# Optimization experiments

Hardware: AMD Instinct MI355X
Metric: run time of the kernel (lower is better)

The kernel has to match this reference:

```python
import jax, jax.numpy as jnp
import numpy as np

NUM_GRAPHS = 64
EPS = 1e-6


def setup_inputs() -> dict:
    key = jax.random.key(0)
    ks = jax.random.split(key, 16)
    S, B, IN, H, N, P_IN, P_OUT = 256, 64, 3, 128, 1_000_000, 8, 32
    src = jax.random.normal(ks[0], (S, B, IN), dtype=jnp.float32)
    src_len = jnp.maximum(jax.random.randint(ks[1], (B,), 0, S + 1), 1).astype(jnp.int32)
    node_x = jax.random.normal(ks[2], (N, H), dtype=jnp.float32)
    # w is a 0/1 node validity mask in the original (float)
    node_w = (jax.random.uniform(ks[3], (N,)) < 0.9).astype(jnp.float32)
    graph_ids = jnp.sort(jax.random.randint(ks[4], (N,), 0, NUM_GRAPHS)).astype(jnp.int32)
    pro_features = jax.random.normal(ks[5], (B, P_IN), dtype=jnp.float32)
    s_in = 1.0 / np.sqrt(IN)
    s_h = 1.0 / np.sqrt(H)
    s_p = 1.0 / np.sqrt(P_IN)
    s_c = 1.0 / np.sqrt(H + P_OUT)
    W_in = jax.random.uniform(ks[6], (IN, H), minval=-s_in, maxval=s_in)
    b_in = jax.random.uniform(ks[7], (H,), minval=-s_in, maxval=s_in)
    W_pred = jax.random.uniform(ks[8], (H, 1), minval=-s_h, maxval=s_h)
    b_pred = jax.random.uniform(ks[9], (1,), minval=-s_h, maxval=s_h)
    W_extra = jax.random.uniform(ks[10], (P_IN, P_OUT), minval=-s_p, maxval=s_p)
    b_extra = jax.random.uniform(ks[11], (P_OUT,), minval=-s_p, maxval=s_p)
    W_hid = jax.random.uniform(ks[12], (P_OUT + H, H), minval=-s_c, maxval=s_c)
    b_hid = jax.random.uniform(ks[13], (H,), minval=-s_c, maxval=s_c)
    return {"src": src, "src_len": src_len, "node_x": node_x, "node_w": node_w,
            "graph_ids": graph_ids, "pro_features": pro_features,
            "W_in": W_in, "b_in": b_in, "W_pred": W_pred, "b_pred": b_pred,
            "W_extra": W_extra, "b_extra": b_extra, "W_hid": W_hid, "b_hid": b_hid}


def mask_graph_log_softmax(lg, w, graph_ids):
    # lg: [N], w: [N], graph_ids: [N] sorted segment ids -> per-graph masked softmax, then log
    maxes = jax.ops.segment_max(lg, graph_ids, num_segments=NUM_GRAPHS)
    x_exp = jnp.exp(lg - maxes[graph_ids]) * w
    x_sum = jax.ops.segment_sum(x_exp, graph_ids, num_segments=NUM_GRAPHS)
    pred = x_exp / (x_sum[graph_ids] + EPS)
    return jnp.log(jnp.clip(pred, EPS, 1.0))


def reference(src, src_len, node_x, node_w, graph_ids, pro_features,
              W_in, b_in, W_pred, b_pred, W_extra, b_extra, W_hid, b_hid):
    S, B = src.shape[0], src.shape[1]
    # mask2d[i, t] = 1 for t < src_len[i]
    mask2d = (jnp.arange(S)[None, :] < src_len[:, None]).astype(src.dtype)  # [B, S]
    h = jnp.tanh(0.0) + src @ W_in + b_in  # [S, B, H]  (fc_in; transformer treated as identity)
    # zero out padded timesteps, then mean over dim 0 (torch.mean divides by S)
    outputs = h * mask2d.T[:, :, None]  # [S, B, H]
    hidden = jnp.mean(outputs, axis=0, keepdims=True)  # [1, B, H]
    # graph segment softmax on node scores
    lg = (node_x @ W_pred + b_pred)[:, 0]  # [N]
    lg_out = mask_graph_log_softmax(lg, node_w, graph_ids)[:, None]  # [N, 1]
    # pro feature fusion
    extra_emb = jnp.tanh(pro_features @ W_extra + b_extra)[None]  # [1, B, P_OUT]
    hidden = jnp.tanh(jnp.concatenate((extra_emb, hidden), axis=2) @ W_hid + b_hid)  # [1, B, H]
    return outputs, hidden, lg_out
```

## Files before the change

kernel.cpp:

```cpp
#include <hip/hip_runtime.h>

#define S_DIM 256
#define B_DIM 64
#define IN_DIM 3
#define H_DIM 128
#define N_NODES 1000000
#define NM1 (N_NODES - 1)
#define P_INF 8
#define P_OUTF 32
#define NUM_GRAPHS 64
#define EPSF 1e-6f

#define OUT_OUTPUTS 0
#define OUT_HIDDEN (S_DIM * B_DIM * H_DIM)
#define OUT_LG (OUT_HIDDEN + B_DIM * H_DIM)

#define NBLK 1024
#define TPB 512
#define RPB 977
#define GSTEP 64
#define SG_SLOTS 6

#define WS_HIDPART 0
#define WS_TBLV (16 * B_DIM * H_DIM)
#define WS_TBLG (WS_TBLV + NBLK * SG_SLOTS)

__global__ void __launch_bounds__(TPB, 8)
main_kernel(const float* __restrict__ src, const int* __restrict__ src_len,
            const float* __restrict__ W_in, const float* __restrict__ b_in,
            const float* __restrict__ node_x, const float* __restrict__ W_pred,
            const float* __restrict__ b_pred, const float* __restrict__ node_w,
            const int* __restrict__ gids,
            float* __restrict__ outputs, float* __restrict__ hid_partial,
            float* __restrict__ lg, float* __restrict__ tblV, int* __restrict__ tblG) {
    __shared__ float sg[SG_SLOTS];
    const int tid = threadIdx.x;
    const int blk = blockIdx.x;
    if (tid < SG_SLOTS) sg[tid] = 0.0f;

    if (blk < 256) {
        int b = blk & 63;
        int chunk = blk >> 6;
        int h = tid & 127;
        int sq = tid >> 7;
        float w0 = W_in[h], w1 = W_in[H_DIM + h], w2 = W_in[2 * H_DIM + h];
        float bi = b_in[h];
        int len = src_len[b];
        float facc = 0.0f;
        int s0 = chunk * 64 + sq * 16;
        for (int s = s0; s < s0 + 16; ++s) {
            const float* sp = src + ((size_t)s * B_DIM + b) * IN_DIM;
            float v = fmaf(sp[0], w0, fmaf(sp[1], w1, fmaf(sp[2], w2, bi)));
            v = (s < len) ? v : 0.0f;
            outputs[((size_t)s * B_DIM + b) * H_DIM + h] = v;
            facc += v;
        }
        hid_partial[((size_t)(chunk * 4 + sq) * B_DIM + b) * H_DIM + h] = facc;
    }
    __syncthreads();

    const int start = blk * RPB;
    const int bend = min(start + RPB, N_NODES);
    const int gfirst = gids[min(start, NM1)];
    const int w = tid >> 6;
    const int lane = tid & 63;
    const int p = lane & 7;
    const int rloc = lane >> 3;

    float4 wch0 = ((const float4*)W_pred)[p];
    float4 wch1 = ((const float4*)W_pred)[p + 8];
    float4 wch2 = ((const float4*)W_pred)[p + 16];
    float4 wch3 = ((const float4*)W_pred)[p + 24];
    const float bp = b_pred[0];

    int curg = -1;
    float acc = 0.0f;

    for (int r0 = start + w * 8; r0 < bend; r0 += GSTEP) {
        int sidx = min(r0 + p, NM1);
        float wv = node_w[sidx];
        int gv = gids[sidx];
        int xrow = min(r0 + rloc, NM1);
        const float4* xb = (const float4*)(node_x + (size_t)xrow * H_DIM);
        float4 x0 = xb[p];
        float4 x1 = xb[p + 8];
        float4 x2 = xb[p + 16];
        float4 x3 = xb[p + 24];
        float s = x0.x * wch0.x + x0.y * wch0.y + x0.z * wch0.z + x0.w * wch0.w;
        s += x1.x * wch1.x + x1.y * wch1.y + x1.z * wch1.z + x1.w * wch1.w;
        s += x2.x * wch2.x + x2.y * wch2.y + x2.z * wch2.z + x2.w * wch2.w;
        s += x3.x * wch3.x + x3.y * wch3.y + x3.z * wch3.z + x3.w * wch3.w;
        s += __shfl_xor(s, 1);
        s += __shfl_xor(s, 2);
        s += __shfl_xor(s, 4);
        float rowsum = __shfl(s, p * 8);
        int myrow = r0 + p;
        if (lane < 8 && myrow < bend) {
            float score = rowsum + bp;
            lg[myrow] = score;
            float xe = __expf(score) * wv;
            if (gv != curg) {
                if (curg >= 0) atomicAdd(&sg[min(curg - gfirst, SG_SLOTS - 1)], acc);
                curg = gv;
                acc = 0.0f;
            }
            acc += xe;
        }
    }
    if (curg >= 0) atomicAdd(&sg[min(curg - gfirst, SG_SLOTS - 1)], acc);
    __syncthreads();
    if (tid < SG_SLOTS) tblV[blk * SG_SLOTS + tid] = sg[tid];
    if (tid == 0) tblG[blk] = gfirst;
}

#define LGOUT_BLOCKS 977

__global__ void __launch_bounds__(256)
finish_kernel(const float* __restrict__ tblV, const int* __restrict__ tblG,
              float* __restrict__ lg, const int* __restrict__ gids,
              const float* __restrict__ node_w,
              const float* __restrict__ pro, const float* __restrict__ W_extra,
              const float* __restrict__ b_extra, const float* __restrict__ W_hid,
              const float* __restrict__ b_hid, const float* __restrict__ hid_partial,
              float* __restrict__ hidden_out) {
    const int tid = threadIdx.x;
    const int blk = blockIdx.x;

    if (blk >= LGOUT_BLOCKS) {
        int b = blk - LGOUT_BLOCKS;
        __shared__ float sh[P_OUTF + H_DIM];
        if (tid < P_OUTF) {
            float a = b_extra[tid];
            #pragma unroll
            for (int k = 0; k < P_INF; ++k) a += pro[b * P_INF + k] * W_extra[k * P_OUTF + tid];
            sh[tid] = tanhf(a);
        }
        if (tid < H_DIM) {
            float m = 0.0f;
            #pragma unroll
            for (int c = 0; c < 16; ++c) m += hid_partial[((size_t)c * B_DIM + b) * H_DIM + tid];
            sh[P_OUTF + tid] = m * (1.0f / S_DIM);
        }
        __syncthreads();
        if (tid < H_DIM) {
            float a = b_hid[tid];
            #pragma unroll 8
            for (int k = 0; k < P_OUTF + H_DIM; ++k) a += sh[k] * W_hid[k * H_DIM + tid];
            hidden_out[(size_t)b * H_DIM + tid] = tanhf(a);
        }
        return;
    }

    __shared__ float gsum[NUM_GRAPHS];
    if (tid < NUM_GRAPHS) gsum[tid] = 0.0f;
    __syncthreads();
    {
        int cg2 = -1;
        float a = 0.0f;
        for (int b = tid * (NBLK / 256); b < (tid + 1) * (NBLK / 256); ++b) {
            int gf = tblG[b];
            #pragma unroll
            for (int slot = 0; slot < SG_SLOTS; ++slot) {
                float v = tblV[b * SG_SLOTS + slot];
                if (v != 0.0f) {
                    int g = min(gf + slot, NUM_GRAPHS - 1);
                    if (g != cg2) {
                        if (cg2 >= 0) atomicAdd(&gsum[cg2], a);
                        cg2 = g;
                        a = 0.0f;
                    }
                    a += v;
                }
            }
        }
        if (cg2 >= 0) atomicAdd(&gsum[cg2], a);
    }
    __syncthreads();

    int n4 = blk * 256 + tid;
    if (n4 >= N_NODES / 4) return;
    float4 l = ((const float4*)lg)[n4];
    float4 w = ((const float4*)node_w)[n4];
    int4 g = ((const int4*)gids)[n4];
    float4 r;
    r.x = __logf(fminf(fmaxf(__expf(l.x) * w.x / (gsum[g.x] + EPSF), EPSF), 1.0f));
    r.y = __logf(fminf(fmaxf(__expf(l.y) * w.y / (gsum[g.y] + EPSF), EPSF), 1.0f));
    r.z = __logf(fminf(fmaxf(__expf(l.z) * w.z / (gsum[g.z] + EPSF), EPSF), 1.0f));
    r.w = __logf(fminf(fmaxf(__expf(l.w) * w.w / (gsum[g.w] + EPSF), EPSF), 1.0f));
    ((float4*)lg)[n4] = r;
}

extern "C" void kernel_launch(void* const* d_in, const int* in_sizes, int n_in,
                              void* d_out, int out_size, void* d_ws, size_t ws_size,
                              hipStream_t stream) {
    const float* src      = (const float*)d_in[0];
    const int*   src_len  = (const int*)d_in[1];
    const float* node_x   = (const float*)d_in[2];
    const float* node_w   = (const float*)d_in[3];
    const int*   gids     = (const int*)d_in[4];
    const float* pro      = (const float*)d_in[5];
    const float* W_in     = (const float*)d_in[6];
    const float* b_in     = (const float*)d_in[7];
    const float* W_pred   = (const float*)d_in[8];
    const float* b_pred   = (const float*)d_in[9];
    const float* W_extra  = (const float*)d_in[10];
    const float* b_extra  = (const float*)d_in[11];
    const float* W_hid    = (const float*)d_in[12];
    const float* b_hid    = (const float*)d_in[13];

    float* out = (float*)d_out;
    float* outputs = out + OUT_OUTPUTS;
    float* hidden  = out + OUT_HIDDEN;
    float* lg      = out + OUT_LG;

    float* ws = (float*)d_ws;
    float* hid_partial = ws + WS_HIDPART;
    float* tblV = ws + WS_TBLV;
    int*   tblG = (int*)(ws + WS_TBLG);

    main_kernel<<<NBLK, TPB, 0, stream>>>(src, src_len, W_in, b_in,
                                          node_x, W_pred, b_pred, node_w, gids,
                                          outputs, hid_partial, lg, tblV, tblG);

    finish_kernel<<<LGOUT_BLOCKS + B_DIM, 256, 0, stream>>>(tblV, tblG, lg, gids, node_w,
                                                            pro, W_extra, b_extra, W_hid,
                                                            b_hid, hid_partial, hidden);
}
```

Before: 123.8 us.

## Fuse main and finish kernels into one cooperative kernel with grid sync

Merges the scoring/projection kernel and the normalization/hidden kernel into a single cooperative launch separated by a grid-wide barrier. The grid size now comes from an occupancy query, and the last 64 blocks compute the hidden output. The node_x reads and the lg reads and writes switch to nontemporal loads and stores. This removes the second launch and inter-kernel gap, at the cost of a grid sync and a simpler per-value atomic reduction of the per-block graph sums.

```diff
diff --git a/kernel.cpp b/kernel.cpp
--- a/kernel.cpp
+++ b/kernel.cpp
@@ -1,4 +1,7 @@
 #include <hip/hip_runtime.h>
+#include <hip/hip_cooperative_groups.h>
+
+namespace cg = cooperative_groups;
 
 #define S_DIM 256
 #define B_DIM 64
@@ -6,6 +9,7 @@
 #define H_DIM 128
 #define N_NODES 1000000
 #define NM1 (N_NODES - 1)
+#define N4_TOTAL (N_NODES / 4)
 #define P_INF 8
 #define P_OUTF 32
 #define NUM_GRAPHS 64
@@ -15,27 +19,35 @@
 #define OUT_HIDDEN (S_DIM * B_DIM * H_DIM)
 #define OUT_LG (OUT_HIDDEN + B_DIM * H_DIM)
 
-#define NBLK 1024
 #define TPB 512
-#define RPB 977
-#define GSTEP 64
+#define NBLK_MAX 1024
 #define SG_SLOTS 6
 
 #define WS_HIDPART 0
 #define WS_TBLV (16 * B_DIM * H_DIM)
-#define WS_TBLG (WS_TBLV + NBLK * SG_SLOTS)
+#define WS_TBLG (WS_TBLV + NBLK_MAX * SG_SLOTS)
+
+typedef float f4v __attribute__((ext_vector_type(4)));
+typedef int i4v __attribute__((ext_vector_type(4)));
 
 __global__ void __launch_bounds__(TPB, 8)
-main_kernel(const float* __restrict__ src, const int* __restrict__ src_len,
-            const float* __restrict__ W_in, const float* __restrict__ b_in,
-            const float* __restrict__ node_x, const float* __restrict__ W_pred,
-            const float* __restrict__ b_pred, const float* __restrict__ node_w,
-            const int* __restrict__ gids,
-            float* __restrict__ outputs, float* __restrict__ hid_partial,
-            float* __restrict__ lg, float* __restrict__ tblV, int* __restrict__ tblG) {
+fused_kernel(const float* __restrict__ src, const int* __restrict__ src_len,
+             const float* __restrict__ W_in, const float* __restrict__ b_in,
+             const float* __restrict__ node_x, const float* __restrict__ W_pred,
+             const float* __restrict__ b_pred, const float* __restrict__ node_w,
+             const int* __restrict__ gids,
+             const float* __restrict__ pro, const float* __restrict__ W_extra,
+             const float* __restrict__ b_extra, const float* __restrict__ W_hid,
+             const float* __restrict__ b_hid,
+             float* __restrict__ outputs, float* __restrict__ hidden_out,
+             float* __restrict__ lg, float* __restrict__ hid_partial,
+             float* __restrict__ tblV, int* __restrict__ tblG, int rpb) {
     __shared__ float sg[SG_SLOTS];
+    __shared__ float gsum[NUM_GRAPHS];
+    __shared__ float sh[P_OUTF + H_DIM];
     const int tid = threadIdx.x;
     const int blk = blockIdx.x;
+    const int nblk = gridDim.x;
     if (tid < SG_SLOTS) sg[tid] = 0.0f;
 
     if (blk < 256) {
@@ -59,33 +71,33 @@
     }
     __syncthreads();
 
-    const int start = blk * RPB;
-    const int bend = min(start + RPB, N_NODES);
+    const int start = blk * rpb;
+    const int bend = min(start + rpb, N_NODES);
     const int gfirst = gids[min(start, NM1)];
     const int w = tid >> 6;
     const int lane = tid & 63;
     const int p = lane & 7;
     const int rloc = lane >> 3;
 
-    float4 wch0 = ((const float4*)W_pred)[p];
-    float4 wch1 = ((const float4*)W_pred)[p + 8];
-    float4 wch2 = ((const float4*)W_pred)[p + 16];
-    float4 wch3 = ((const float4*)W_pred)[p + 24];
+    f4v wch0 = ((const f4v*)W_pred)[p];
+    f4v wch1 = ((const f4v*)W_pred)[p + 8];
+    f4v wch2 = ((const f4v*)W_pred)[p + 16];
+    f4v wch3 = ((const f4v*)W_pred)[p + 24];
     const float bp = b_pred[0];
 
     int curg = -1;
     float acc = 0.0f;
 
-    for (int r0 = start + w * 8; r0 < bend; r0 += GSTEP) {
+    for (int r0 = start + w * 8; r0 < bend; r0 += 64) {
         int sidx = min(r0 + p, NM1);
         float wv = node_w[sidx];
         int gv = gids[sidx];
         int xrow = min(r0 + rloc, NM1);
-        const float4* xb = (const float4*)(node_x + (size_t)xrow * H_DIM);
-        float4 x0 = xb[p];
-        float4 x1 = xb[p + 8];
-        float4 x2 = xb[p + 16];
-        float4 x3 = xb[p + 24];
+        const f4v* xb = (const f4v*)(node_x + (size_t)xrow * H_DIM);
+        f4v x0 = __builtin_nontemporal_load(xb + p);
+        f4v x1 = __builtin_nontemporal_load(xb + p + 8);
+        f4v x2 = __builtin_nontemporal_load(xb + p + 16);
+        f4v x3 = __builtin_nontemporal_load(xb + p + 24);
         float s = x0.x * wch0.x + x0.y * wch0.y + x0.z * wch0.z + x0.w * wch0.w;
         s += x1.x * wch1.x + x1.y * wch1.y + x1.z * wch1.z + x1.w * wch1.w;
         s += x2.x * wch2.x + x2.y * wch2.y + x2.z * wch2.z + x2.w * wch2.w;
@@ -97,7 +109,7 @@
         int myrow = r0 + p;
         if (lane < 8 && myrow < bend) {
             float score = rowsum + bp;
-            lg[myrow] = score;
+            __builtin_nontemporal_store(score, &lg[myrow]);
             float xe = __expf(score) * wv;
             if (gv != curg) {
                 if (curg >= 0) atomicAdd(&sg[min(curg - gfirst, SG_SLOTS - 1)], acc);
@@ -111,24 +123,11 @@
     __syncthreads();
     if (tid < SG_SLOTS) tblV[blk * SG_SLOTS + tid] = sg[tid];
     if (tid == 0) tblG[blk] = gfirst;
-}
-
-#define LGOUT_BLOCKS 977
-
-__global__ void __launch_bounds__(256)
-finish_kernel(const float* __restrict__ tblV, const int* __restrict__ tblG,
-              float* __restrict__ lg, const int* __restrict__ gids,
-              const float* __restrict__ node_w,
-              const float* __restrict__ pro, const float* __restrict__ W_extra,
-              const float* __restrict__ b_extra, const float* __restrict__ W_hid,
-              const float* __restrict__ b_hid, const float* __restrict__ hid_partial,
-              float* __restrict__ hidden_out) {
-    const int tid = threadIdx.x;
-    const int blk = blockIdx.x;
-
-    if (blk >= LGOUT_BLOCKS) {
-        int b = blk - LGOUT_BLOCKS;
-        __shared__ float sh[P_OUTF + H_DIM];
+
+    cg::this_grid().sync();
+
+    if (blk >= nblk - 64) {
+        int b = blk - (nblk - 64);
         if (tid < P_OUTF) {
             float a = b_extra[tid];
             #pragma unroll
@@ -151,43 +150,32 @@
         return;
     }
 
-    __shared__ float gsum[NUM_GRAPHS];
+    if (blk * TPB >= N4_TOTAL) return;
+
     if (tid < NUM_GRAPHS) gsum[tid] = 0.0f;
     __syncthreads();
-    {
-        int cg2 = -1;
-        float a = 0.0f;
-        for (int b = tid * (NBLK / 256); b < (tid + 1) * (NBLK / 256); ++b) {
-            int gf = tblG[b];
-            #pragma unroll
-            for (int slot = 0; slot < SG_SLOTS; ++slot) {
-                float v = tblV[b * SG_SLOTS + slot];
-                if (v != 0.0f) {
-                    int g = min(gf + slot, NUM_GRAPHS - 1);
-                    if (g != cg2) {
-                        if (cg2 >= 0) atomicAdd(&gsum[cg2], a);
-                        cg2 = g;
-                        a = 0.0f;
-                    }
-                    a += v;
-                }
-            }
-        }
-        if (cg2 >= 0) atomicAdd(&gsum[cg2], a);
-    }
-    __syncthreads();
-
-    int n4 = blk * 256 + tid;
-    if (n4 >= N_NODES / 4) return;
-    float4 l = ((const float4*)lg)[n4];
-    float4 w = ((const float4*)node_w)[n4];
-    int4 g = ((const int4*)gids)[n4];
-    float4 r;
-    r.x = __logf(fminf(fmaxf(__expf(l.x) * w.x / (gsum[g.x] + EPSF), EPSF), 1.0f));
-    r.y = __logf(fminf(fmaxf(__expf(l.y) * w.y / (gsum[g.y] + EPSF), EPSF), 1.0f));
-    r.z = __logf(fminf(fmaxf(__expf(l.z) * w.z / (gsum[g.z] + EPSF), EPSF), 1.0f));
-    r.w = __logf(fminf(fmaxf(__expf(l.w) * w.w / (gsum[g.w] + EPSF), EPSF), 1.0f));
-    ((float4*)lg)[n4] = r;
+    for (int b = tid; b < nblk; b += TPB) {
+        int gf = tblG[b];
+        #pragma unroll
+        for (int slot = 0; slot < SG_SLOTS; ++slot) {
+            float v = tblV[b * SG_SLOTS + slot];
+            if (v != 0.0f) atomicAdd(&gsum[min(gf + slot, NUM_GRAPHS - 1)], v);
+        }
+    }
+    __syncthreads();
+
+    int stride = (nblk - 64) * TPB;
+    for (int n4 = blk * TPB + tid; n4 < N4_TOTAL; n4 += stride) {
+        f4v l = __builtin_nontemporal_load((const f4v*)lg + n4);
+        f4v wq = __builtin_nontemporal_load((const f4v*)node_w + n4);
+        i4v g = __builtin_nontemporal_load((const i4v*)gids + n4);
+        f4v r;
+        r.x = __logf(fminf(fmaxf(__expf(l.x) * wq.x / (gsum[g.x] + EPSF), EPSF), 1.0f));
+        r.y = __logf(fminf(fmaxf(__expf(l.y) * wq.y / (gsum[g.y] + EPSF), EPSF), 1.0f));
+        r.z = __logf(fminf(fmaxf(__expf(l.z) * wq.z / (gsum[g.z] + EPSF), EPSF), 1.0f));
+        r.w = __logf(fminf(fmaxf(__expf(l.w) * wq.w / (gsum[g.w] + EPSF), EPSF), 1.0f));
+        __builtin_nontemporal_store(r, (f4v*)lg + n4);
+    }
 }
 
 extern "C" void kernel_launch(void* const* d_in, const int* in_sizes, int n_in,
@@ -218,11 +206,22 @@
     float* tblV = ws + WS_TBLV;
     int*   tblG = (int*)(ws + WS_TBLG);
 
-    main_kernel<<<NBLK, TPB, 0, stream>>>(src, src_len, W_in, b_in,
-                                          node_x, W_pred, b_pred, node_w, gids,
-                                          outputs, hid_partial, lg, tblV, tblG);
-
-    finish_kernel<<<LGOUT_BLOCKS + B_DIM, 256, 0, stream>>>(tblV, tblG, lg, gids, node_w,
-                                                            pro, W_extra, b_extra, W_hid,
-                                                            b_hid, hid_partial, hidden);
+    int nb_per_cu = 0;
+    hipOccupancyMaxActiveBlocksPerMultiprocessor(&nb_per_cu, (const void*)fused_kernel,
+                                                 TPB, 0);
+    int nblk = nb_per_cu * 256;
+    if (nblk > NBLK_MAX) nblk = NBLK_MAX;
+    if (nblk < 320) nblk = 320;
+    int rpb = (N_NODES + nblk - 1) / nblk;
+
+    void* args[] = {
+        (void*)&src, (void*)&src_len, (void*)&W_in, (void*)&b_in,
+        (void*)&node_x, (void*)&W_pred, (void*)&b_pred, (void*)&node_w,
+        (void*)&gids, (void*)&pro, (void*)&W_extra, (void*)&b_extra,
+        (void*)&W_hid, (void*)&b_hid,
+        (void*)&outputs, (void*)&hidden, (void*)&lg, (void*)&hid_partial,
+        (void*)&tblV, (void*)&tblG, (void*)&rpb
+    };
+    hipLaunchCooperativeKernel((const void*)fused_kernel, dim3(nblk), dim3(TPB),
+                               args, 0, stream);
 }
```

Result: slower. 183.5 us (+48.2%).
